# Optimization experiments

Measured on AMD Instinct MI355X. Metric: run time of the kernel, lower is better.

Reference implementation:

```python
import jax, jax.numpy as jnp
import numpy as np

B, T, EMB_D, HEAD = 8, 2048, 1024, 128


def setup_inputs() -> dict:
    key = jax.random.key(0)
    ks = jax.random.split(key, 7)
    s = 1.0 / np.sqrt(EMB_D)
    return {
        "inputs": jax.random.normal(ks[0], (B, T, EMB_D), dtype=jnp.float32),
        "Wk": jax.random.uniform(ks[1], (EMB_D, HEAD), jnp.float32, -s, s),
        "bk": jax.random.uniform(ks[2], (HEAD,), jnp.float32, -s, s),
        "Wq": jax.random.uniform(ks[3], (EMB_D, HEAD), jnp.float32, -s, s),
        "bq": jax.random.uniform(ks[4], (HEAD,), jnp.float32, -s, s),
        "Wv": jax.random.uniform(ks[5], (EMB_D, HEAD), jnp.float32, -s, s),
        "bv": jax.random.uniform(ks[6], (HEAD,), jnp.float32, -s, s),
    }


def reference(inputs, Wk, bk, Wq, bq, Wv, bv):
    # inputs: [B, T, C]
    Bq, Tq, _ = inputs.shape
    k = inputs @ Wk + bk  # [B, T, H]
    q = inputs @ Wq + bq
    v = inputs @ Wv + bv
    scale = HEAD ** -0.5
    weights = jnp.einsum("bth,bsh->bts", q, k) * scale  # [B, T, T]
    causal = jnp.tril(jnp.ones((Tq, Tq), dtype=bool))
    weights = jnp.where(causal, weights, -jnp.inf)
    # NOTE: original code applies softmax over dim=1 (the query axis), faithfully reproduced
    weights = jax.nn.softmax(weights, axis=1)
    return jnp.einsum("bts,bsh->bth", weights, v)  # [B, T, H]
```

## Files before the change

### kernel.cpp

```cpp
#include <hip/hip_runtime.h>
#include <hip/hip_bf16.h>

#define T_SEQ 2048
#define NBATCH 8
#define EMB 1024
#define HD 128

typedef _Float16 f16_t;
typedef _Float16 f16x8 __attribute__((ext_vector_type(8)));
typedef _Float16 f16x4 __attribute__((ext_vector_type(4)));
typedef float f32x4 __attribute__((ext_vector_type(4)));


__device__ __forceinline__ void g2l(const f16_t* g, f16_t* l) {
    __builtin_amdgcn_global_load_lds(
        (const __attribute__((address_space(1))) unsigned int*)g,
        (__attribute__((address_space(3))) unsigned int*)l, 16, 0, 0);
}

__global__ __launch_bounds__(256) void prep(
    const float* __restrict__ Wk, const float* __restrict__ bk,
    const float* __restrict__ Wq, const float* __restrict__ bq,
    const float* __restrict__ Wv, const float* __restrict__ bv,
    f16_t* __restrict__ w2, float* __restrict__ biasc) {
    int n = blockIdx.x;
    int t = threadIdx.x;
    const float scale = 0.08838834764831845f;
    const float* W; const float* bias; float sc; int col;
    if (n < 128)      { W = Wq; bias = bq; sc = scale; col = n; }
    else if (n < 256) { W = Wk; bias = bk; sc = 1.0f;  col = n - 128; }
    else              { W = Wv; bias = bv; sc = 1.0f;  col = n - 256; }
    if (t < 128) {
        int k0 = t * 8;
        f16x8 v;
        #pragma unroll
        for (int i = 0; i < 8; ++i) v[i] = (f16_t)(W[(size_t)(k0 + i) * HD + col] * sc);
        *(f16x8*)&w2[(size_t)(n >> 4) * 16384 + (size_t)(k0 >> 3) * 128 + (n & 15) * 8] = v;
    }
    if (t == 0) biasc[n] = bias[col] * sc;
}

__global__ __launch_bounds__(256) void qkv_gemm(
    const float* __restrict__ X, const f16_t* __restrict__ w2,
    const float* __restrict__ biasc,
    f16_t* __restrict__ q2, f16_t* __restrict__ k2, f16_t* __restrict__ v2) {
    __shared__ f16_t Xs[2][64 * 72];
    __shared__ __align__(16) f16_t Bl[2][8 * 1024];

    int bid = blockIdx.x;
    int r8 = bid & 7, g = bid >> 3;
    int band = (g / 3) * 8 + r8;
    int i = g % 3;
    int m0 = band * 64, n0 = i * 128;
    int tid = threadIdx.x;
    int lane = tid & 63, w = tid >> 6;
    int quad = lane >> 4, l15 = lane & 15;
    int msub = (w & 1) * 32, nsub = (w >> 1) * 64;

    int srow = tid >> 2;
    int scg  = (tid & 3) * 16;

    const float* xrow = X + (size_t)(m0 + srow) * EMB + scg;
    const f16_t* bbase = w2 + (size_t)(n0 >> 4) * 16384;

    f32x4 acc[2][4] = {};
    float4 pf[4];

    auto loadA = [&](int kc) {
        #pragma unroll
        for (int u = 0; u < 4; ++u) pf[u] = *(const float4*)(xrow + kc * 64 + u * 4);
    };
    auto stageB = [&](int kc, int buf) {
        const f16_t* bsrc = bbase + (size_t)kc * 1024;
        #pragma unroll
        for (int ii = 0; ii < 4; ++ii) {
            int D = tid * 16 + ii * 4096;
            g2l(bsrc + (size_t)(D >> 11) * 16384 + ((D & 2047) >> 1),
                &Bl[buf][D >> 1]);
        }
    };
    auto stageA = [&](int buf) {
        union { f16_t h[8]; uint4 u4; } p0, p1;
        p0.h[0] = (f16_t)pf[0].x; p0.h[1] = (f16_t)pf[0].y;
        p0.h[2] = (f16_t)pf[0].z; p0.h[3] = (f16_t)pf[0].w;
        p0.h[4] = (f16_t)pf[1].x; p0.h[5] = (f16_t)pf[1].y;
        p0.h[6] = (f16_t)pf[1].z; p0.h[7] = (f16_t)pf[1].w;
        p1.h[0] = (f16_t)pf[2].x; p1.h[1] = (f16_t)pf[2].y;
        p1.h[2] = (f16_t)pf[2].z; p1.h[3] = (f16_t)pf[2].w;
        p1.h[4] = (f16_t)pf[3].x; p1.h[5] = (f16_t)pf[3].y;
        p1.h[6] = (f16_t)pf[3].z; p1.h[7] = (f16_t)pf[3].w;
        *(uint4*)&Xs[buf][srow * 72 + scg] = p0.u4;
        *(uint4*)&Xs[buf][srow * 72 + scg + 8] = p1.u4;
    };
    auto compute = [&](int buf) {
        #pragma unroll
        for (int ks = 0; ks < 2; ++ks) {
            f16x8 afr0 = *(const f16x8*)&Xs[buf][(msub + l15) * 72 + ks * 32 + quad * 8];
            f16x8 afr1 = *(const f16x8*)&Xs[buf][(msub + 16 + l15) * 72 + ks * 32 + quad * 8];
            #pragma unroll
            for (int nf = 0; nf < 4; ++nf) {
                int ntl = (nsub >> 4) + nf;
                f16x8 bfr = *(const f16x8*)&Bl[buf][ntl * 1024 + (ks * 4 + quad) * 128 + l15 * 8];
                acc[0][nf] = __builtin_amdgcn_mfma_f32_16x16x32_f16(afr0, bfr, acc[0][nf], 0, 0, 0);
                acc[1][nf] = __builtin_amdgcn_mfma_f32_16x16x32_f16(afr1, bfr, acc[1][nf], 0, 0, 0);
            }
        }
    };

    loadA(0);
    stageB(0, 0);
    stageA(0);
    __syncthreads();

    for (int kc = 0; kc < 16; ++kc) {
        int cur = kc & 1, nxt = cur ^ 1;
        if (kc + 1 < 16) {
            loadA(kc + 1);
            stageB(kc + 1, nxt);
        }
        compute(cur);
        if (kc + 1 < 16) stageA(nxt);
        __syncthreads();
    }

    #pragma unroll
    for (int nf = 0; nf < 4; ++nf) {
        int ng = n0 + nsub + nf * 16 + l15;
        float bval = biasc[ng];
        #pragma unroll
        for (int mf = 0; mf < 2; ++mf) {
            int rowg = m0 + msub + mf * 16 + quad * 4;
            f32x4 a = acc[mf][nf];
            if (ng < 256) {
                f16_t* dst = (ng < 128) ? q2 : k2;
                int c = ng & 127;
                #pragma unroll
                for (int r = 0; r < 4; ++r) {
                    int row = rowg + r;
                    dst[(size_t)(row >> 4) * 2048 + (c >> 3) * 128 + (row & 15) * 8 + (c & 7)]
                        = (f16_t)(a[r] + bval);
                }
            } else {
                int h = ng - 256;
                f16x4 hv;
                #pragma unroll
                for (int r = 0; r < 4; ++r) hv[r] = (f16_t)(a[r] + bval);
                *(f16x4*)&v2[(size_t)(rowg >> 3) * 1024 + h * 8 + (rowg & 7)] = hv;
            }
        }
    }
}

__global__ __launch_bounds__(256, 4) void col_stats(
    const f16_t* __restrict__ q2, const f16_t* __restrict__ k2,
    float* __restrict__ colsum) {
    int bid = blockIdx.x;
    int b = bid & 7;
    int item = 143 - (bid >> 3);
    int cg = 0, slab = 0, cum = 0;
    for (int c = 0; c < 32; ++c) {
        int n = (32 - c + 3) >> 2;
        if (item < cum + n) { cg = c; slab = item - cum; break; }
        cum += n;
    }
    int tc0 = cg + slab * 4, tc1 = min(tc0 + 4, 32);

    int tid = threadIdx.x, lane = tid & 63, w = tid >> 6;
    int quad = lane >> 4, l15 = lane & 15;
    int brow = b * 128;
    size_t base = (size_t)b * T_SEQ;

    f16x8 bfrs[4][4];
    #pragma unroll
    for (int st = 0; st < 4; ++st) {
        const f16_t* kt = k2 + (size_t)(brow + cg * 4 + st) * 2048 + l15 * 8;
        #pragma unroll
        for (int kf = 0; kf < 4; ++kf)
            bfrs[st][kf] = *(const f16x8*)(kt + (kf * 4 + quad) * 128);
    }

    float lacc[4] = {0.f, 0.f, 0.f, 0.f};

    for (int tc = tc0; tc < tc1; ++tc) {
        int tb = tc * 64;
        f16x8 afr[4];
        const f16_t* qt = q2 + (size_t)(brow + tc * 4 + w) * 2048 + l15 * 8;
        #pragma unroll
        for (int kf = 0; kf < 4; ++kf)
            afr[kf] = *(const f16x8*)(qt + (kf * 4 + quad) * 128);
        #pragma unroll
        for (int st = 0; st < 4; ++st) {
            f32x4 s = {};
            #pragma unroll
            for (int kf = 0; kf < 4; ++kf)
                s = __builtin_amdgcn_mfma_f32_16x16x32_f16(afr[kf], bfrs[st][kf], s, 0, 0, 0);
            int scol = cg * 64 + st * 16 + l15;
            #pragma unroll
            for (int r = 0; r < 4; ++r) {
                int t = tb + w * 16 + quad * 4 + r;
                if (t >= scol) lacc[st] += __expf(s[r]);
            }
        }
    }

    #pragma unroll
    for (int st = 0; st < 4; ++st) {
        float v = lacc[st];
        v += __shfl_xor(v, 16, 64);
        v += __shfl_xor(v, 32, 64);
        if (quad == 0) atomicAdd(&colsum[base + cg * 64 + st * 16 + l15], v);
    }
}

__global__ __launch_bounds__(256, 3) void attn_out(
    const f16_t* __restrict__ q2, const f16_t* __restrict__ k2,
    const f16_t* __restrict__ v2, const float* __restrict__ colsum,
    float* __restrict__ out) {
    __shared__ __align__(16) f16_t Pl[2][32 * 72];

    int bid = blockIdx.x;
    int b = bid & 7;
    int item = 159 - (bid >> 3);
    int g = 0, slab = 0, cum = 0;
    for (int gg = 0; gg < 64; ++gg) {
        int n = (((gg >> 1) + 1) + 7) >> 3;
        if (item < cum + n) { g = gg; slab = item - cum; break; }
        cum += n;
    }
    int nch = (g >> 1) + 1;
    int c0 = slab * 8, c1 = min(c0 + 8, nch);
    int trow = g * 32;

    int tid = threadIdx.x, lane = tid & 63, w = tid >> 6;
    int quad = lane >> 4, l15 = lane & 15;
    int brow = b * 128;
    size_t base = (size_t)b * T_SEQ;

    f16x8 qfr[2][4];
    #pragma unroll
    for (int tt = 0; tt < 2; ++tt) {
        const f16_t* qt = q2 + (size_t)(brow + 2 * g + tt) * 2048 + l15 * 8;
        #pragma unroll
        for (int kf = 0; kf < 4; ++kf)
            qfr[tt][kf] = *(const f16x8*)(qt + (kf * 4 + quad) * 128);
    }

    f32x4 o[2][2] = {};

    f16x8 kA[4], kB[4];
    f16x8 vA[2][2], vB[2][2];
    float csA, csB;

    auto loadKVc = [&](int c, f16x8 (&k)[4], f16x8 (&v)[2][2], float& cs) {
        const f16_t* kt = k2 + (size_t)(brow + c * 4 + w) * 2048 + l15 * 8;
        #pragma unroll
        for (int kf = 0; kf < 4; ++kf)
            k[kf] = *(const f16x8*)(kt + (kf * 4 + quad) * 128);
        const f16_t* vt = v2 + ((size_t)(base + c * 64) >> 3) * 1024;
        #pragma unroll
        for (int kf2 = 0; kf2 < 2; ++kf2)
            #pragma unroll
            for (int hh = 0; hh < 2; ++hh)
                v[kf2][hh] = *(const f16x8*)&vt[(kf2 * 4 + quad) * 1024 +
                                                (w * 32 + hh * 16 + l15) * 8];
        cs = colsum[base + c * 64 + w * 16 + l15];
    };
    auto qkt = [&](int c, f16x8 (&k)[4], float cs, int pb) {
        float iv = 1.0f / cs;
        int scol = c * 64 + w * 16 + l15;
        #pragma unroll
        for (int tt = 0; tt < 2; ++tt) {
            f32x4 s = {};
            #pragma unroll
            for (int kf = 0; kf < 4; ++kf)
                s = __builtin_amdgcn_mfma_f32_16x16x32_f16(qfr[tt][kf], k[kf], s, 0, 0, 0);
            #pragma unroll
            for (int r = 0; r < 4; ++r) {
                int t = trow + tt * 16 + quad * 4 + r;
                float pv = (t >= scol) ? __expf(s[r]) * iv : 0.f;
                Pl[pb][(tt * 16 + quad * 4 + r) * 72 + w * 16 + l15] = (f16_t)pv;
            }
        }
    };
    auto pvstep = [&](f16x8 (&v)[2][2], int pb) {
        #pragma unroll
        for (int kf2 = 0; kf2 < 2; ++kf2) {
            f16x8 pa0 = *(const f16x8*)&Pl[pb][(l15) * 72 + kf2 * 32 + quad * 8];
            f16x8 pa1 = *(const f16x8*)&Pl[pb][(16 + l15) * 72 + kf2 * 32 + quad * 8];
            #pragma unroll
            for (int hh = 0; hh < 2; ++hh) {
                o[0][hh] = __builtin_amdgcn_mfma_f32_16x16x32_f16(pa0, v[kf2][hh], o[0][hh], 0, 0, 0);
                o[1][hh] = __builtin_amdgcn_mfma_f32_16x16x32_f16(pa1, v[kf2][hh], o[1][hh], 0, 0, 0);
            }
        }
    };

    int c = c0;
    loadKVc(c, kA, vA, csA);
    for (; c + 1 < c1; c += 2) {
        qkt(c, kA, csA, 0);
        __syncthreads();
        loadKVc(c + 1, kB, vB, csB);
        pvstep(vA, 0);
        qkt(c + 1, kB, csB, 1);
        __syncthreads();
        if (c + 2 < c1) loadKVc(c + 2, kA, vA, csA);
        pvstep(vB, 1);
    }
    if (c < c1) {
        qkt(c, kA, csA, 0);
        __syncthreads();
        pvstep(vA, 0);
    }

    #pragma unroll
    for (int tt = 0; tt < 2; ++tt)
        #pragma unroll
        for (int hh = 0; hh < 2; ++hh)
            #pragma unroll
            for (int r = 0; r < 4; ++r)
                atomicAdd(&out[(base + trow + tt * 16 + quad * 4 + r) * HD + w * 32 + hh * 16 + l15],
                          o[tt][hh][r]);
}

extern "C" void kernel_launch(void* const* d_in, const int* in_sizes, int n_in,
                              void* d_out, int out_size, void* d_ws, size_t ws_size,
                              hipStream_t stream) {
    const float* X  = (const float*)d_in[0];
    const float* Wk = (const float*)d_in[1];
    const float* bk = (const float*)d_in[2];
    const float* Wq = (const float*)d_in[3];
    const float* bq = (const float*)d_in[4];
    const float* Wv = (const float*)d_in[5];
    const float* bv = (const float*)d_in[6];
    float* out = (float*)d_out;

    char* ws = (char*)d_ws;
    const size_t W2_B    = 24 * 16384 * 2;
    const size_t BIAS_B  = 2048;
    const size_t QKV_B   = (size_t)NBATCH * T_SEQ * HD * 2;
    f16_t* w2     = (f16_t*)ws;
    float* biasc  = (float*)(ws + W2_B);
    f16_t* q2     = (f16_t*)(ws + W2_B + BIAS_B);
    f16_t* k2     = (f16_t*)(ws + W2_B + BIAS_B + QKV_B);
    f16_t* v2     = (f16_t*)(ws + W2_B + BIAS_B + 2 * QKV_B);
    float* colsum = (float*)(ws + W2_B + BIAS_B + 3 * QKV_B);

    hipMemsetAsync(out, 0, (size_t)NBATCH * T_SEQ * HD * sizeof(float), stream);
    hipMemsetAsync(colsum, 0, (size_t)NBATCH * T_SEQ * sizeof(float), stream);

    prep<<<dim3(384), dim3(256), 0, stream>>>(Wk, bk, Wq, bq, Wv, bv, w2, biasc);
    qkv_gemm<<<dim3(768), dim3(256), 0, stream>>>(X, w2, biasc, q2, k2, v2);
    col_stats<<<dim3(1152), dim3(256), 0, stream>>>(q2, k2, colsum);
    attn_out<<<dim3(1280), dim3(256), 0, stream>>>(q2, k2, v2, colsum, out);
}
```

Before: 174.0 us.

## Enlarge QKV GEMM tiles and read weight fragments directly from global memory

Retiles the QKV projection GEMM from 64x128 to 128x192 tiles per block, with a 4x6 MFMA accumulator grid per wave and 256 blocks instead of 768. This cuts redundant reads of X across the three N tiles. The shared-memory staging of the weight operand is removed, and B fragments are loaded straight from global memory (likely L2-resident) inside the MFMA loop. The trade-offs are higher register pressure, fewer blocks than CUs for occupancy, and global-load latency on the B operand with no prefetch.

```diff
diff --git a/kernel.cpp b/kernel.cpp
--- a/kernel.cpp
+++ b/kernel.cpp
@@ -44,91 +44,77 @@
     const float* __restrict__ X, const f16_t* __restrict__ w2,
     const float* __restrict__ biasc,
     f16_t* __restrict__ q2, f16_t* __restrict__ k2, f16_t* __restrict__ v2) {
-    __shared__ f16_t Xs[2][64 * 72];
-    __shared__ __align__(16) f16_t Bl[2][8 * 1024];
+    __shared__ f16_t Xs[2][128 * 72];
 
     int bid = blockIdx.x;
-    int r8 = bid & 7, g = bid >> 3;
-    int band = (g / 3) * 8 + r8;
-    int i = g % 3;
-    int m0 = band * 64, n0 = i * 128;
+    int band = bid >> 1, i = bid & 1;
+    int m0 = band * 128, n0 = i * 192;
     int tid = threadIdx.x;
     int lane = tid & 63, w = tid >> 6;
     int quad = lane >> 4, l15 = lane & 15;
-    int msub = (w & 1) * 32, nsub = (w >> 1) * 64;
-
-    int srow = tid >> 2;
-    int scg  = (tid & 3) * 16;
+    int msub = (w & 1) * 64, nsub = (w >> 1) * 96;
+
+    int srow = tid >> 1;
+    int scg  = (tid & 1) * 32;
 
     const float* xrow = X + (size_t)(m0 + srow) * EMB + scg;
-    const f16_t* bbase = w2 + (size_t)(n0 >> 4) * 16384;
-
-    f32x4 acc[2][4] = {};
-    float4 pf[4];
+    int ntb = (n0 + nsub) >> 4;
+
+    f32x4 acc[4][6] = {};
+    float4 pf[8];
 
     auto loadA = [&](int kc) {
         #pragma unroll
-        for (int u = 0; u < 4; ++u) pf[u] = *(const float4*)(xrow + kc * 64 + u * 4);
-    };
-    auto stageB = [&](int kc, int buf) {
-        const f16_t* bsrc = bbase + (size_t)kc * 1024;
-        #pragma unroll
-        for (int ii = 0; ii < 4; ++ii) {
-            int D = tid * 16 + ii * 4096;
-            g2l(bsrc + (size_t)(D >> 11) * 16384 + ((D & 2047) >> 1),
-                &Bl[buf][D >> 1]);
-        }
+        for (int u = 0; u < 8; ++u) pf[u] = *(const float4*)(xrow + kc * 64 + u * 4);
     };
     auto stageA = [&](int buf) {
-        union { f16_t h[8]; uint4 u4; } p0, p1;
-        p0.h[0] = (f16_t)pf[0].x; p0.h[1] = (f16_t)pf[0].y;
-        p0.h[2] = (f16_t)pf[0].z; p0.h[3] = (f16_t)pf[0].w;
-        p0.h[4] = (f16_t)pf[1].x; p0.h[5] = (f16_t)pf[1].y;
-        p0.h[6] = (f16_t)pf[1].z; p0.h[7] = (f16_t)pf[1].w;
-        p1.h[0] = (f16_t)pf[2].x; p1.h[1] = (f16_t)pf[2].y;
-        p1.h[2] = (f16_t)pf[2].z; p1.h[3] = (f16_t)pf[2].w;
-        p1.h[4] = (f16_t)pf[3].x; p1.h[5] = (f16_t)pf[3].y;
-        p1.h[6] = (f16_t)pf[3].z; p1.h[7] = (f16_t)pf[3].w;
-        *(uint4*)&Xs[buf][srow * 72 + scg] = p0.u4;
-        *(uint4*)&Xs[buf][srow * 72 + scg + 8] = p1.u4;
-    };
-    auto compute = [&](int buf) {
+        #pragma unroll
+        for (int p = 0; p < 4; ++p) {
+            union { f16_t h[8]; uint4 u4; } pk;
+            pk.h[0] = (f16_t)pf[2 * p].x;     pk.h[1] = (f16_t)pf[2 * p].y;
+            pk.h[2] = (f16_t)pf[2 * p].z;     pk.h[3] = (f16_t)pf[2 * p].w;
+            pk.h[4] = (f16_t)pf[2 * p + 1].x; pk.h[5] = (f16_t)pf[2 * p + 1].y;
+            pk.h[6] = (f16_t)pf[2 * p + 1].z; pk.h[7] = (f16_t)pf[2 * p + 1].w;
+            *(uint4*)&Xs[buf][srow * 72 + scg + p * 8] = pk.u4;
+        }
+    };
+    auto compute = [&](int kc, int buf) {
         #pragma unroll
         for (int ks = 0; ks < 2; ++ks) {
-            f16x8 afr0 = *(const f16x8*)&Xs[buf][(msub + l15) * 72 + ks * 32 + quad * 8];
-            f16x8 afr1 = *(const f16x8*)&Xs[buf][(msub + 16 + l15) * 72 + ks * 32 + quad * 8];
-            #pragma unroll
-            for (int nf = 0; nf < 4; ++nf) {
-                int ntl = (nsub >> 4) + nf;
-                f16x8 bfr = *(const f16x8*)&Bl[buf][ntl * 1024 + (ks * 4 + quad) * 128 + l15 * 8];
-                acc[0][nf] = __builtin_amdgcn_mfma_f32_16x16x32_f16(afr0, bfr, acc[0][nf], 0, 0, 0);
-                acc[1][nf] = __builtin_amdgcn_mfma_f32_16x16x32_f16(afr1, bfr, acc[1][nf], 0, 0, 0);
+            f16x8 afr[4];
+            #pragma unroll
+            for (int mf = 0; mf < 4; ++mf)
+                afr[mf] = *(const f16x8*)&Xs[buf][(msub + mf * 16 + l15) * 72 + ks * 32 + quad * 8];
+            #pragma unroll
+            for (int nf = 0; nf < 6; ++nf) {
+                f16x8 bfr = *(const f16x8*)&w2[(size_t)(ntb + nf) * 16384 +
+                    (size_t)(kc * 8 + ks * 4 + quad) * 128 + l15 * 8];
+                #pragma unroll
+                for (int mf = 0; mf < 4; ++mf)
+                    acc[mf][nf] = __builtin_amdgcn_mfma_f32_16x16x32_f16(
+                        afr[mf], bfr, acc[mf][nf], 0, 0, 0);
             }
         }
     };
 
     loadA(0);
-    stageB(0, 0);
     stageA(0);
     __syncthreads();
 
     for (int kc = 0; kc < 16; ++kc) {
-        int cur = kc & 1, nxt = cur ^ 1;
-        if (kc + 1 < 16) {
-            loadA(kc + 1);
-            stageB(kc + 1, nxt);
-        }
-        compute(cur);
-        if (kc + 1 < 16) stageA(nxt);
+        int cur = kc & 1;
+        if (kc + 1 < 16) loadA(kc + 1);
+        compute(kc, cur);
+        if (kc + 1 < 16) stageA(cur ^ 1);
         __syncthreads();
     }
 
     #pragma unroll
-    for (int nf = 0; nf < 4; ++nf) {
+    for (int nf = 0; nf < 6; ++nf) {
         int ng = n0 + nsub + nf * 16 + l15;
         float bval = biasc[ng];
         #pragma unroll
-        for (int mf = 0; mf < 2; ++mf) {
+        for (int mf = 0; mf < 4; ++mf) {
             int rowg = m0 + msub + mf * 16 + quad * 4;
             f32x4 a = acc[mf][nf];
             if (ng < 256) {
@@ -350,7 +336,7 @@
     hipMemsetAsync(colsum, 0, (size_t)NBATCH * T_SEQ * sizeof(float), stream);
 
     prep<<<dim3(384), dim3(256), 0, stream>>>(Wk, bk, Wq, bq, Wv, bv, w2, biasc);
-    qkv_gemm<<<dim3(768), dim3(256), 0, stream>>>(X, w2, biasc, q2, k2, v2);
+    qkv_gemm<<<dim3(256), dim3(256), 0, stream>>>(X, w2, biasc, q2, k2, v2);
     col_stats<<<dim3(1152), dim3(256), 0, stream>>>(q2, k2, colsum);
     attn_out<<<dim3(1280), dim3(256), 0, stream>>>(q2, k2, v2, colsum, out);
 }
```

Result: slower. 195.9 us (+12.6%).
